# Kernel optimization log

Measured on AMD Instinct MI355X. Metric: run time of the kernel, lower is better.

The kernel has to match this reference:

```python
import jax, jax.numpy as jnp
import numpy as np


def _grid_sample(feat, grid):
    """Bilinear grid_sample, zeros padding, align_corners=False (torch default).
    feat: (B,C,H,W); grid: (B,Hg,Wg,2) normalized to [-1,1]. Returns (B,C,Hg,Wg)."""
    B, C, H, W = feat.shape
    gx, gy = grid[..., 0], grid[..., 1]
    ix = ((gx + 1.0) * W - 1.0) * 0.5
    iy = ((gy + 1.0) * H - 1.0) * 0.5
    x0 = jnp.floor(ix)
    y0 = jnp.floor(iy)
    wx = ix - x0
    wy = iy - y0

    def sample_one(f, x0, y0, wx, wy):
        def gather(xi, yi):
            valid = (xi >= 0) & (xi <= W - 1) & (yi >= 0) & (yi <= H - 1)
            xc = jnp.clip(xi, 0, W - 1).astype(jnp.int32)
            yc = jnp.clip(yi, 0, H - 1).astype(jnp.int32)
            return f[:, yc, xc] * valid[None].astype(f.dtype)
        v00 = gather(x0, y0)
        v01 = gather(x0 + 1, y0)
        v10 = gather(x0, y0 + 1)
        v11 = gather(x0 + 1, y0 + 1)
        return (v00 * (1 - wx) * (1 - wy) + v01 * wx * (1 - wy)
                + v10 * (1 - wx) * wy + v11 * wx * wy)

    return jax.vmap(sample_one)(feat, x0, y0, wx, wy)


def _homo_warp(src_feat, depth_hypo, src_K, src_c2w, ref_K, ref_c2w):
    """src_feat (B,C,H,W), depth_hypo (B,D,H,W) -> warped (B,C,D,H,W)."""
    B, C, H, W = src_feat.shape
    D = depth_hypo.shape[1]
    src_w2c = jnp.linalg.inv(src_c2w)
    ref_w2c = jnp.linalg.inv(ref_c2w)
    # Faithful to torch: clone w2c, overwrite top-left 3x3 with intrinsics.
    src_K4 = src_w2c.at[:, :3, :3].set(src_K)
    ref_K4 = ref_w2c.at[:, :3, :3].set(ref_K)
    src_proj = src_K4 @ src_w2c
    ref_proj = ref_K4 @ ref_w2c
    proj = src_proj @ jnp.linalg.inv(ref_proj)
    rot = proj[:, :3, :3]                      # (B,3,3)
    trans = proj[:, :3, 3]                     # (B,3)
    y, x = jnp.meshgrid(jnp.arange(H, dtype=src_feat.dtype),
                        jnp.arange(W, dtype=src_feat.dtype), indexing='ij')
    xyz = jnp.stack([x.ravel(), y.ravel(), jnp.ones(H * W, src_feat.dtype)], 0)  # (3,HW)
    rot_xyz = jnp.einsum('bij,jn->bin', rot, xyz)                                 # (B,3,HW)
    d = depth_hypo.reshape(B, 1, D, H * W)
    proj_xyz = rot_xyz[:, :, None, :] * d + trans[:, :, None, None]               # (B,3,D,HW)
    proj_xy = proj_xyz[:, :2] / proj_xyz[:, 2:3]
    gx = proj_xy[:, 0] / ((W - 1) / 2.0) - 1.0
    gy = proj_xy[:, 1] / ((H - 1) / 2.0) - 1.0
    grid = jax.lax.stop_gradient(jnp.stack([gx, gy], -1).reshape(B, D * H, W, 2))
    warped = _grid_sample(src_feat, grid)                                          # (B,C,D*H,W)
    return warped.reshape(B, C, D, H, W)


def _unfold5(x):
    """F.unfold(k=5,p=2) reshaped: (B,C,H,W) -> (B,C,25,H,W); k = dy*5+dx."""
    B, C, H, W = x.shape
    xp = jnp.pad(x, ((0, 0), (0, 0), (2, 2), (2, 2)))
    return jnp.stack([xp[:, :, dy:dy + H, dx:dx + W]
                      for dy in range(5) for dx in range(5)], axis=2)


def _cost_aggregation(cost, ref_feat, depth_hypo):
    B, D, H, W = cost.shape
    CENTER = 12  # index of 5x5 window center
    cost_nb = _unfold5(cost)                                           # (B,D,25,H,W)
    depth_nb = jax.lax.stop_gradient(_unfold5(depth_hypo))             # (B,D,25,H,W)
    w_depth = jax.nn.softmax(-jnp.abs(depth_nb - depth_nb[:, :, CENTER:CENTER + 1]), axis=2)
    feat_nb = jax.lax.stop_gradient(_unfold5(ref_feat))                # (B,C,25,H,W)
    w_feat = jnp.sum(feat_nb[:, :, CENTER:CENTER + 1] * feat_nb, axis=1, keepdims=True)
    w_feat = jax.nn.softmax(jnp.broadcast_to(w_feat, (B, D, 25, H, W)), axis=2)
    weight = jax.lax.stop_gradient(jax.nn.softmax(w_depth * w_feat, axis=2))
    return jnp.sum(cost_nb * weight, axis=2)                           # (B,D,H,W)


def setup_inputs() -> dict:
    key = jax.random.key(0)
    V, B, C, D, H, W = 3, 2, 32, 32, 128, 160
    k1, k2 = jax.random.split(key)
    features = jax.random.normal(k1, (V, B, C, H, W), jnp.float32)
    uncertainty = jax.random.normal(k2, (B, H, W), jnp.float32)
    K = np.array([[float(W), 0.0, (W - 1) / 2.0],
                  [0.0, float(W), (H - 1) / 2.0],
                  [0.0, 0.0, 1.0]], np.float32)
    intrinsics = np.broadcast_to(K, (V, B, 3, 3)).copy()
    c2w = np.tile(np.eye(4, dtype=np.float32), (V, B, 1, 1))
    for v in range(1, V):
        ang = 0.05 * v
        R = np.array([[np.cos(ang), 0.0, np.sin(ang)],
                      [0.0, 1.0, 0.0],
                      [-np.sin(ang), 0.0, np.cos(ang)]], np.float32)
        c2w[v, :, :3, :3] = R
        c2w[v, :, 0, 3] = 0.2 * v
    depth_vals = jnp.asarray(np.linspace(2.0, 10.0, D, dtype=np.float32))
    depth_hypo = jnp.broadcast_to(depth_vals[None, :, None, None], (B, D, H, W)) + 0.0
    return {
        'features': features,
        'intrinsics': jnp.asarray(intrinsics),
        'cam_to_world': jnp.asarray(c2w),
        'depth_hypo': depth_hypo,
        'uncertainty': uncertainty,
    }


def reference(features, intrinsics, cam_to_world, depth_hypo, uncertainty):
    ref_feat = features[0]                                             # (B,C,H,W)
    V = features.shape[0]
    unc = jax.nn.sigmoid(uncertainty)[:, None, None]                   # (B,1,1,H,W)
    pairwise = []
    for v in range(1, V):
        warped = _homo_warp(features[v], depth_hypo,
                            intrinsics[v], cam_to_world[v],
                            intrinsics[0], cam_to_world[0])            # (B,C,D,H,W)
        c = jnp.sum(ref_feat[:, :, None] * warped, axis=1, keepdims=True)  # correlation
        pairwise.append(c * unc)
    cost = jnp.min(jnp.stack(pairwise, 0), axis=0)[:, 0]               # (B,D,H,W)
    agg = _cost_aggregation(cost, ref_feat, depth_hypo)
    prob = jax.nn.softmax(agg, axis=1)
    return jnp.sum(prob * depth_hypo, axis=1)                          # (B,H,W)
```

## Files before the change

kernel.cpp:

```cpp
#include <hip/hip_runtime.h>
#include <hip/hip_fp16.h>
#include <math.h>

#define V_ 3
#define B_ 2
#define C_ 32
#define D_ 32
#define H_ 128
#define W_ 160
#define HW_ (H_*W_)
#define NPIX_ (B_*H_*W_)
#define NCOST_ (B_*D_*H_*W_)

struct H8 { __half2 h[4]; };

__device__ __forceinline__ void inv4(const double* m, double* o) {
    double inv[16];
    inv[0]  =  m[5]*m[10]*m[15] - m[5]*m[11]*m[14] - m[9]*m[6]*m[15] + m[9]*m[7]*m[14] + m[13]*m[6]*m[11] - m[13]*m[7]*m[10];
    inv[4]  = -m[4]*m[10]*m[15] + m[4]*m[11]*m[14] + m[8]*m[6]*m[15] - m[8]*m[7]*m[14] - m[12]*m[6]*m[11] + m[12]*m[7]*m[10];
    inv[8]  =  m[4]*m[9]*m[15]  - m[4]*m[11]*m[13] - m[8]*m[5]*m[15] + m[8]*m[7]*m[13] + m[12]*m[5]*m[11] - m[12]*m[7]*m[9];
    inv[12] = -m[4]*m[9]*m[14]  + m[4]*m[10]*m[13] + m[8]*m[5]*m[14] - m[8]*m[6]*m[13] - m[12]*m[5]*m[10] + m[12]*m[6]*m[9];
    inv[1]  = -m[1]*m[10]*m[15] + m[1]*m[11]*m[14] + m[9]*m[2]*m[15] - m[9]*m[3]*m[14] - m[13]*m[2]*m[11] + m[13]*m[3]*m[10];
    inv[5]  =  m[0]*m[10]*m[15] - m[0]*m[11]*m[14] - m[8]*m[2]*m[15] + m[8]*m[3]*m[14] + m[12]*m[2]*m[11] - m[12]*m[3]*m[10];
    inv[9]  = -m[0]*m[9]*m[15]  + m[0]*m[11]*m[13] + m[8]*m[1]*m[15] - m[8]*m[3]*m[13] - m[12]*m[1]*m[11] + m[12]*m[3]*m[9];
    inv[13] =  m[0]*m[9]*m[14]  - m[0]*m[10]*m[13] - m[8]*m[1]*m[14] + m[8]*m[2]*m[13] + m[12]*m[1]*m[10] - m[12]*m[2]*m[9];
    inv[2]  =  m[1]*m[6]*m[15]  - m[1]*m[7]*m[14]  - m[5]*m[2]*m[15] + m[5]*m[3]*m[14] + m[13]*m[2]*m[7]  - m[13]*m[3]*m[6];
    inv[6]  = -m[0]*m[6]*m[15]  + m[0]*m[7]*m[14]  + m[4]*m[2]*m[15] - m[4]*m[3]*m[14] - m[12]*m[2]*m[7]  + m[12]*m[3]*m[6];
    inv[10] =  m[0]*m[5]*m[15]  - m[0]*m[7]*m[13]  - m[4]*m[1]*m[15] + m[4]*m[3]*m[13] + m[12]*m[1]*m[7]  - m[12]*m[3]*m[5];
    inv[14] = -m[0]*m[5]*m[14]  + m[0]*m[6]*m[13]  + m[4]*m[1]*m[14] - m[4]*m[2]*m[13] - m[12]*m[1]*m[6]  + m[12]*m[2]*m[5];
    inv[3]  = -m[1]*m[6]*m[11]  + m[1]*m[7]*m[10]  + m[5]*m[2]*m[11] - m[5]*m[3]*m[10] - m[9]*m[2]*m[7]   + m[9]*m[3]*m[6];
    inv[7]  =  m[0]*m[6]*m[11]  - m[0]*m[7]*m[10]  - m[4]*m[2]*m[11] + m[4]*m[3]*m[10] + m[8]*m[2]*m[7]   - m[8]*m[3]*m[6];
    inv[11] = -m[0]*m[5]*m[11]  + m[0]*m[7]*m[9]   + m[4]*m[1]*m[11] - m[4]*m[3]*m[9]  - m[8]*m[1]*m[7]   + m[8]*m[3]*m[5];
    inv[15] =  m[0]*m[5]*m[10]  - m[0]*m[6]*m[9]   - m[4]*m[1]*m[10] + m[4]*m[2]*m[9]  + m[8]*m[1]*m[6]   - m[8]*m[2]*m[5];
    double det = m[0]*inv[0] + m[1]*inv[4] + m[2]*inv[8] + m[3]*inv[12];
    det = 1.0 / det;
    for (int i = 0; i < 16; i++) o[i] = inv[i] * det;
}

__device__ __forceinline__ void mm4(const double* A, const double* Bm, double* Cm) {
    for (int r = 0; r < 4; r++)
        for (int c = 0; c < 4; c++) {
            double s = 0.0;
            for (int k = 0; k < 4; k++) s += A[r*4+k] * Bm[k*4+c];
            Cm[r*4+c] = s;
        }
}

__global__ void __launch_bounds__(256) transproj_kernel(const float* __restrict__ feat,
                                                        const float* __restrict__ K,
                                                        const float* __restrict__ c2w,
                                                        float* __restrict__ refT,
                                                        __half* __restrict__ fh,
                                                        float* __restrict__ proj_out) {
    int bid = blockIdx.x;
    int tid = threadIdx.x;
    if (bid == V_ * B_ * H_ * (W_ / 32)) {
        int t = tid;
        if (t >= (V_-1) * B_) return;
        int vv = t / B_;
        int b  = t % B_;
        int v  = vv + 1;
        double sc[16], rc[16];
        for (int i = 0; i < 16; i++) {
            sc[i] = (double)c2w[((size_t)v * B_ + b) * 16 + i];
            rc[i] = (double)c2w[((size_t)0 * B_ + b) * 16 + i];
        }
        double sw[16], rw[16];
        inv4(sc, sw);
        inv4(rc, rw);
        double sK[16], rK[16];
        for (int i = 0; i < 16; i++) { sK[i] = sw[i]; rK[i] = rw[i]; }
        for (int r = 0; r < 3; r++)
            for (int c = 0; c < 3; c++) {
                sK[r*4+c] = (double)K[((size_t)v * B_ + b) * 9 + r*3 + c];
                rK[r*4+c] = (double)K[((size_t)0 * B_ + b) * 9 + r*3 + c];
            }
        double sp[16], rp[16], rpi[16], P[16];
        mm4(sK, sw, sp);
        mm4(rK, rw, rp);
        inv4(rp, rpi);
        mm4(sp, rpi, P);
        float* o = proj_out + (size_t)t * 12;
        for (int r = 0; r < 3; r++)
            for (int c = 0; c < 3; c++) o[r*3+c] = (float)P[r*4+c];
        for (int r = 0; r < 3; r++) o[9+r] = (float)P[r*4+3];
        return;
    }
    __shared__ float lds[32][33];
    int xt = bid % (W_ / 32);
    int y  = (bid / (W_ / 32)) % H_;
    int vb = bid / ((W_ / 32) * H_);
    int v = vb >> 1, b = vb & 1;
    int x0 = xt * 32;
    int xl = tid & 31;
    int ch = tid >> 5;
#pragma unroll
    for (int it = 0; it < 4; it++) {
        int c = it * 8 + ch;
        lds[c][xl] = feat[((size_t)(vb * C_ + c) * H_ + y) * W_ + x0 + xl];
    }
    __syncthreads();
    int c4 = tid & 7;
    int xw = tid >> 3;
    float4 o;
    o.x = lds[c4*4+0][xw];
    o.y = lds[c4*4+1][xw];
    o.z = lds[c4*4+2][xw];
    o.w = lds[c4*4+3][xw];
    size_t pix = (size_t)(b * H_ + y) * W_ + x0 + xw;
    if (v == 0) {
        *(float4*)(refT + pix * C_ + c4 * 4) = o;
    } else {
        uint2 st;
        __half2 p0 = __floats2half2_rn(o.x, o.y);
        __half2 p1 = __floats2half2_rn(o.z, o.w);
        st.x = *(unsigned int*)&p0;
        st.y = *(unsigned int*)&p1;
        size_t dst = ((size_t)((v - 1) * B_ + b) * HW_ + (y * W_ + x0 + xw));
        *(uint2*)((unsigned short*)fh + dst * C_ + c4 * 4) = st;
    }
}

union SmemU {
    struct { float4 lw[2][256]; int4 lo[2][256]; } c;
    float4 wbox[5 * 36 * 8];
};
__global__ void __launch_bounds__(256, 4) costwfeat_kernel(const float* __restrict__ refT,
                                                           const __half* __restrict__ fh,
                                                           const float* __restrict__ depth,
                                                           const float* __restrict__ unc,
                                                           const float* __restrict__ proj,
                                                           float* __restrict__ cost,
                                                           float* __restrict__ wfeat) {
    __shared__ SmemU sm;
    int tid = threadIdx.x;
    int bid = blockIdx.x;
    const int blocksPerDt = NPIX_ / 32;

    if (bid < 4 * blocksPerDt) {
        int dt      = bid / blocksPerDt;
        int pixbase = (bid % blocksPerDt) * 32;
        int d0 = dt * 8;
        {
            int pixl = tid & 31;
            int dl   = tid >> 5;
            int pix = pixbase + pixl;
            int x = pix % W_;
            int y = (pix / W_) % H_;
            int b = pix / HW_;
            float dep = depth[((b * D_ + d0 + dl) * H_ + y) * W_ + x];
            float fx = (float)x, fy = (float)y;
#pragma unroll
            for (int v = 0; v < 2; v++) {
                const float* P = proj + ((size_t)v * B_ + b) * 12;
                float rx = P[0]*fx + P[1]*fy + P[2];
                float ry = P[3]*fx + P[4]*fy + P[5];
                float rz = P[6]*fx + P[7]*fy + P[8];
                float px = rx * dep + P[9];
                float py = ry * dep + P[10];
                float pz = rz * dep + P[11];
                float inv_pz = 1.0f / pz;
                float t0 = px * inv_pz;
                float t1 = py * inv_pz;
                float gx = t0 / ((W_ - 1) * 0.5f) - 1.0f;
                float gy = t1 / ((H_ - 1) * 0.5f) - 1.0f;
                float ix = ((gx + 1.0f) * W_ - 1.0f) * 0.5f;
                float iy = ((gy + 1.0f) * H_ - 1.0f) * 0.5f;
                float x0f = floorf(ix), y0f = floorf(iy);
                float wx = ix - x0f, wy = iy - y0f;
                int x0 = (int)x0f, y0 = (int)y0f;
                int x1 = x0 + 1, y1 = y0 + 1;
                bool vx0 = (x0 >= 0) && (x0 <= W_ - 1);
                bool vx1 = (x1 >= 0) && (x1 <= W_ - 1);
                bool vy0 = (y0 >= 0) && (y0 <= H_ - 1);
                bool vy1 = (y1 >= 0) && (y1 <= H_ - 1);
                float4 w;
                w.x = (vx0 && vy0) ? (1.0f - wx) * (1.0f - wy) : 0.0f;
                w.y = (vx1 && vy0) ? wx * (1.0f - wy) : 0.0f;
                w.z = (vx0 && vy1) ? (1.0f - wx) * wy : 0.0f;
                w.w = (vx1 && vy1) ? wx * wy : 0.0f;
                int xc0 = min(max(x0, 0), W_ - 1), xc1 = min(max(x1, 0), W_ - 1);
                int yc0 = min(max(y0, 0), H_ - 1), yc1 = min(max(y1, 0), H_ - 1);
                int4 o;
                o.x = (yc0 * W_ + xc0) << 6;
                o.y = (yc0 * W_ + xc1) << 6;
                o.z = (yc1 * W_ + xc0) << 6;
                o.w = (yc1 * W_ + xc1) << 6;
                sm.c.lw[v][tid] = w;
                sm.c.lo[v][tid] = o;
            }
        }
        __syncthreads();

        int c8 = tid & 3;
        int g  = (tid >> 2) & 31;
        int h  = tid >> 7;
        int pix = pixbase + g;
        int x = pix % W_;
        int y = (pix / W_) % H_;
        int b = pix / HW_;

        const float4* rT4 = (const float4*)refT;
        const float4 r0 = rT4[(size_t)pix * 8 + c8 * 2];
        const float4 r1 = rT4[(size_t)pix * 8 + c8 * 2 + 1];
        const char* bA = (const char*)fh + ((size_t)(0 * B_ + b) * HW_) * 64 + c8 * 16;
        const char* bB = (const char*)fh + ((size_t)(1 * B_ + b) * HW_) * 64 + c8 * 16;

        float u = unc[pix];
        float sig = 1.0f / (1.0f + __expf(-u));

        float myres = 0.0f;
#pragma unroll
        for (int i = 0; i < 4; i++) {
            int e = (h * 4 + i) * 32 + g;
            float pv[2];
#pragma unroll
            for (int v = 0; v < 2; v++) {
                float4 Wt = sm.c.lw[v][e];
                int4   Of = sm.c.lo[v][e];
                const char* base = v ? bB : bA;
                H8 a  = *(const H8*)(base + Of.x);
                H8 bq = *(const H8*)(base + Of.y);
                H8 cq = *(const H8*)(base + Of.z);
                H8 eq = *(const H8*)(base + Of.w);
                __half2 w0 = __float2half2_rn(Wt.x);
                __half2 w1 = __float2half2_rn(Wt.y);
                __half2 w2 = __float2half2_rn(Wt.z);
                __half2 w3 = __float2half2_rn(Wt.w);
                __half2 acc0 = __hmul2(w0, a.h[0]);
                __half2 acc1 = __hmul2(w0, a.h[1]);
                __half2 acc2 = __hmul2(w0, a.h[2]);
                __half2 acc3 = __hmul2(w0, a.h[3]);
                acc0 = __hfma2(w1, bq.h[0], acc0);
                acc1 = __hfma2(w1, bq.h[1], acc1);
                acc2 = __hfma2(w1, bq.h[2], acc2);
                acc3 = __hfma2(w1, bq.h[3], acc3);
                acc0 = __hfma2(w2, cq.h[0], acc0);
                acc1 = __hfma2(w2, cq.h[1], acc1);
                acc2 = __hfma2(w2, cq.h[2], acc2);
                acc3 = __hfma2(w2, cq.h[3], acc3);
                acc0 = __hfma2(w3, eq.h[0], acc0);
                acc1 = __hfma2(w3, eq.h[1], acc1);
                acc2 = __hfma2(w3, eq.h[2], acc2);
                acc3 = __hfma2(w3, eq.h[3], acc3);
                float2 f0 = __half22float2(acc0);
                float2 f1 = __half22float2(acc1);
                float2 f2 = __half22float2(acc2);
                float2 f3 = __half22float2(acc3);
                float p = r0.x*f0.x + r0.y*f0.y + r0.z*f1.x + r0.w*f1.y
                        + r1.x*f2.x + r1.y*f2.y + r1.z*f3.x + r1.w*f3.y;
                p += __shfl_xor(p, 1);
                p += __shfl_xor(p, 2);
                pv[v] = p;
            }
            float r = fminf(pv[0], pv[1]) * sig;
            if (c8 == i) myres = r;
        }
        cost[((b * D_ + d0 + h * 4 + c8) * H_ + y) * W_ + x] = myres;
    } else {
        int wbid = bid - 4 * blocksPerDt;
        int g  = tid >> 3;
        int c4 = tid & 7;
        int pixbase = wbid * 32;
        int x0 = pixbase % W_;
        int yb = (pixbase / W_) % H_;
        int b  = pixbase / HW_;
        const float4* rT4 = (const float4*)refT;

        for (int e = tid; e < 5 * 36 * 8; e += 256) {
            int ent = e >> 3, q = e & 7;
            int ry = ent / 36, rx = ent - ry * 36;
            int yy = yb + ry - 2, xx = x0 + rx - 2;
            float4 val = make_float4(0.f, 0.f, 0.f, 0.f);
            if (yy >= 0 && yy < H_ && xx >= 0 && xx < W_)
                val = rT4[(size_t)((b * H_ + yy) * W_ + xx) * 8 + q];
            sm.wbox[e] = val;
        }
        __syncthreads();

        const float4 r = sm.wbox[(2 * 36 + g + 2) * 8 + c4];
        float logit[25];
#pragma unroll
        for (int k = 0; k < 25; k++) {
            int dy = k / 5, dx = k % 5;
            float4 q = sm.wbox[(dy * 36 + g + dx) * 8 + c4];
            float p = r.x*q.x + r.y*q.y + r.z*q.z + r.w*q.w;
            p += __shfl_xor(p, 1);
            p += __shfl_xor(p, 2);
            p += __shfl_xor(p, 4);
            logit[k] = p;
        }
        float m = logit[0];
#pragma unroll
        for (int k = 1; k < 25; k++) m = fmaxf(m, logit[k]);
        float s = 0.0f;
#pragma unroll
        for (int k = 0; k < 25; k++) { logit[k] = __expf(logit[k] - m); s += logit[k]; }
        float inv_s = 1.0f / s;
        int pix = pixbase + g;
#pragma unroll
        for (int t = 0; t < 3; t++) {
            int k = c4 + 8 * t;
            wfeat[(size_t)k * NPIX_ + pix] = logit[k] * inv_s;
        }
        if (c4 == 0) wfeat[(size_t)24 * NPIX_ + pix] = logit[24] * inv_s;
    }
}

__global__ void __launch_bounds__(256, 4) aggfinal_kernel(const float* __restrict__ depth,
                                                          const float* __restrict__ cost,
                                                          const float* __restrict__ wfeat,
                                                          float* __restrict__ out) {
    __shared__ float wf[25][33];
    __shared__ float aval[D_][33];
    __shared__ float dval[D_][33];
    int tid = threadIdx.x;
    int xl = tid & 31;
    int dl = tid >> 5;
    int bid = blockIdx.x;
    int xt = bid % (W_ / 32);
    int by = bid / (W_ / 32);
    int y = by % H_;
    int b = by / H_;
    int x = xt * 32 + xl;

    for (int li = tid; li < 25 * 32; li += 256) {
        int k  = li >> 5;
        int pp = li & 31;
        wf[k][pp] = wfeat[(size_t)k * NPIX_ + (b * H_ + y) * W_ + xt * 32 + pp];
    }
    __syncthreads();

#pragma unroll
    for (int i = 0; i < 4; i++) {
        int d = dl * 4 + i;
        size_t dslice = (size_t)(b * D_ + d) * HW_;
        float dc = depth[dslice + y * W_ + x];

        float wd[25];
        float s1 = 0.0f;
#pragma unroll
        for (int k = 0; k < 25; k++) {
            int dy = k / 5 - 2, dx = k % 5 - 2;
            int ny = y + dy, nx = x + dx;
            bool ok = (ny >= 0 && ny < H_ && nx >= 0 && nx < W_);
            float nd = ok ? depth[dslice + ny * W_ + nx] : 0.0f;
            float e = __expf(-fabsf(nd - dc));
            wd[k] = e;
            s1 += e;
        }
        float inv_s1 = 1.0f / s1;

        float s2 = 0.0f;
        float acc = 0.0f;
#pragma unroll
        for (int k = 0; k < 25; k++) {
            float e = __expf((wd[k] * inv_s1) * wf[k][xl]);
            s2 += e;
            int dy = k / 5 - 2, dx = k % 5 - 2;
            int ny = y + dy, nx = x + dx;
            bool ok = (ny >= 0 && ny < H_ && nx >= 0 && nx < W_);
            float cv = ok ? cost[dslice + ny * W_ + nx] : 0.0f;
            acc += cv * e;
        }
        aval[d][xl] = acc / s2;
        dval[d][xl] = dc;
    }
    __syncthreads();

    if (tid < 32) {
        float m = -1e30f;
#pragma unroll
        for (int dd = 0; dd < D_; dd++) m = fmaxf(m, aval[dd][tid]);
        float s = 0.0f, ws = 0.0f;
#pragma unroll
        for (int dd = 0; dd < D_; dd++) {
            float e = __expf(aval[dd][tid] - m);
            s += e;
            ws += e * dval[dd][tid];
        }
        out[(b * H_ + y) * W_ + xt * 32 + tid] = ws / s;
    }
}

extern "C" void kernel_launch(void* const* d_in, const int* in_sizes, int n_in,
                              void* d_out, int out_size, void* d_ws, size_t ws_size,
                              hipStream_t stream) {
    const float* features = (const float*)d_in[0];
    const float* intr     = (const float*)d_in[1];
    const float* c2w      = (const float*)d_in[2];
    const float* depth    = (const float*)d_in[3];
    const float* unc      = (const float*)d_in[4];
    float* out = (float*)d_out;

    float*  ws    = (float*)d_ws;
    float*  refT  = ws;
    __half* fh    = (__half*)(refT + (size_t)B_ * HW_ * C_);
    float*  cost  = (float*)(fh + (size_t)2 * B_ * HW_ * C_);
    float*  wfeat = cost + NCOST_;
    float*  proj  = wfeat + (size_t)25 * NPIX_;

    hipLaunchKernelGGL(transproj_kernel, dim3(V_ * B_ * H_ * (W_ / 32) + 1), dim3(256), 0, stream,
                       features, intr, c2w, refT, fh, proj);
    hipLaunchKernelGGL(costwfeat_kernel, dim3((NPIX_ * 4) / 32 + NPIX_ / 32), dim3(256), 0, stream,
                       refT, fh, depth, unc, proj, cost, wfeat);
    hipLaunchKernelGGL(aggfinal_kernel, dim3(NPIX_ / 32), dim3(256), 0, stream,
                       depth, cost, wfeat, out);
}
```

Baseline: 70.44 us.

## Store reference features in fp16 and use packed fdot2 for correlations

The reference view's features are now stored as fp16 in the same transposed buffer as the source views, not as fp32. The cost kernel computes per-corner dot products with the v_dot2 fp32-accumulate instruction and applies the bilinear weights afterwards, instead of interpolating in fp16 and then dotting in fp32. The aggregation-weight path also reads fp16 neighbours into a halved shared-memory box, and the launch bound raises target occupancy to 8 blocks per unit. This cuts memory traffic and shared memory but lowers precision of the reference features, and the correlation changes from one interpolated dot product to four dot products.

Measured after the change: 74.23 us. 5.4% more time.

```diff
diff --git a/kernel.cpp b/kernel.cpp
--- a/kernel.cpp
+++ b/kernel.cpp
@@ -13,6 +13,17 @@
 #define NCOST_ (B_*D_*H_*W_)
 
 struct H8 { __half2 h[4]; };
+struct H4 { __half2 h[2]; };
+
+typedef _Float16 hv2 __attribute__((ext_vector_type(2)));
+__device__ __forceinline__ float fdot2f(__half2 a, __half2 b, float c) {
+#if __has_builtin(__builtin_amdgcn_fdot2)
+    return __builtin_amdgcn_fdot2(*(hv2*)&a, *(hv2*)&b, c, false);
+#else
+    float2 fa = __half22float2(a), fb = __half22float2(b);
+    return c + fa.x * fb.x + fa.y * fb.y;
+#endif
+}
 
 __device__ __forceinline__ void inv4(const double* m, double* o) {
     double inv[16];
@@ -49,7 +60,6 @@
 __global__ void __launch_bounds__(256) transproj_kernel(const float* __restrict__ feat,
                                                         const float* __restrict__ K,
                                                         const float* __restrict__ c2w,
-                                                        float* __restrict__ refT,
                                                         __half* __restrict__ fh,
                                                         float* __restrict__ proj_out) {
     int bid = blockIdx.x;
@@ -90,7 +100,6 @@
     int xt = bid % (W_ / 32);
     int y  = (bid / (W_ / 32)) % H_;
     int vb = bid / ((W_ / 32) * H_);
-    int v = vb >> 1, b = vb & 1;
     int x0 = xt * 32;
     int xl = tid & 31;
     int ch = tid >> 5;
@@ -107,26 +116,20 @@
     o.y = lds[c4*4+1][xw];
     o.z = lds[c4*4+2][xw];
     o.w = lds[c4*4+3][xw];
-    size_t pix = (size_t)(b * H_ + y) * W_ + x0 + xw;
-    if (v == 0) {
-        *(float4*)(refT + pix * C_ + c4 * 4) = o;
-    } else {
-        uint2 st;
-        __half2 p0 = __floats2half2_rn(o.x, o.y);
-        __half2 p1 = __floats2half2_rn(o.z, o.w);
-        st.x = *(unsigned int*)&p0;
-        st.y = *(unsigned int*)&p1;
-        size_t dst = ((size_t)((v - 1) * B_ + b) * HW_ + (y * W_ + x0 + xw));
-        *(uint2*)((unsigned short*)fh + dst * C_ + c4 * 4) = st;
-    }
+    uint2 st;
+    __half2 p0 = __floats2half2_rn(o.x, o.y);
+    __half2 p1 = __floats2half2_rn(o.z, o.w);
+    st.x = *(unsigned int*)&p0;
+    st.y = *(unsigned int*)&p1;
+    size_t dst = (size_t)vb * HW_ + (y * W_ + x0 + xw);
+    *(uint2*)((unsigned short*)fh + dst * C_ + c4 * 4) = st;
 }
 
 union SmemU {
     struct { float4 lw[2][256]; int4 lo[2][256]; } c;
-    float4 wbox[5 * 36 * 8];
+    H4 wbox2[5 * 36 * 8];
 };
-__global__ void __launch_bounds__(256, 4) costwfeat_kernel(const float* __restrict__ refT,
-                                                           const __half* __restrict__ fh,
+__global__ void __launch_bounds__(256, 8) costwfeat_kernel(const __half* __restrict__ fh,
                                                            const float* __restrict__ depth,
                                                            const float* __restrict__ unc,
                                                            const float* __restrict__ proj,
@@ -200,11 +203,9 @@
         int y = (pix / W_) % H_;
         int b = pix / HW_;
 
-        const float4* rT4 = (const float4*)refT;
-        const float4 r0 = rT4[(size_t)pix * 8 + c8 * 2];
-        const float4 r1 = rT4[(size_t)pix * 8 + c8 * 2 + 1];
-        const char* bA = (const char*)fh + ((size_t)(0 * B_ + b) * HW_) * 64 + c8 * 16;
-        const char* bB = (const char*)fh + ((size_t)(1 * B_ + b) * HW_) * 64 + c8 * 16;
+        const H8 rh = *(const H8*)((const char*)fh + (size_t)pix * 64 + c8 * 16);
+        const char* bA = (const char*)fh + ((size_t)(NPIX_ + b * HW_)) * 64 + c8 * 16;
+        const char* bB = (const char*)fh + ((size_t)(2 * NPIX_ + b * HW_)) * 64 + c8 * 16;
 
         float u = unc[pix];
         float sig = 1.0f / (1.0f + __expf(-u));
@@ -223,32 +224,15 @@
                 H8 bq = *(const H8*)(base + Of.y);
                 H8 cq = *(const H8*)(base + Of.z);
                 H8 eq = *(const H8*)(base + Of.w);
-                __half2 w0 = __float2half2_rn(Wt.x);
-                __half2 w1 = __float2half2_rn(Wt.y);
-                __half2 w2 = __float2half2_rn(Wt.z);
-                __half2 w3 = __float2half2_rn(Wt.w);
-                __half2 acc0 = __hmul2(w0, a.h[0]);
-                __half2 acc1 = __hmul2(w0, a.h[1]);
-                __half2 acc2 = __hmul2(w0, a.h[2]);
-                __half2 acc3 = __hmul2(w0, a.h[3]);
-                acc0 = __hfma2(w1, bq.h[0], acc0);
-                acc1 = __hfma2(w1, bq.h[1], acc1);
-                acc2 = __hfma2(w1, bq.h[2], acc2);
-                acc3 = __hfma2(w1, bq.h[3], acc3);
-                acc0 = __hfma2(w2, cq.h[0], acc0);
-                acc1 = __hfma2(w2, cq.h[1], acc1);
-                acc2 = __hfma2(w2, cq.h[2], acc2);
-                acc3 = __hfma2(w2, cq.h[3], acc3);
-                acc0 = __hfma2(w3, eq.h[0], acc0);
-                acc1 = __hfma2(w3, eq.h[1], acc1);
-                acc2 = __hfma2(w3, eq.h[2], acc2);
-                acc3 = __hfma2(w3, eq.h[3], acc3);
-                float2 f0 = __half22float2(acc0);
-                float2 f1 = __half22float2(acc1);
-                float2 f2 = __half22float2(acc2);
-                float2 f3 = __half22float2(acc3);
-                float p = r0.x*f0.x + r0.y*f0.y + r0.z*f1.x + r0.w*f1.y
-                        + r1.x*f2.x + r1.y*f2.y + r1.z*f3.x + r1.w*f3.y;
+                float d00 = 0.f, d01 = 0.f, d10 = 0.f, d11 = 0.f;
+#pragma unroll
+                for (int j = 0; j < 4; j++) {
+                    d00 = fdot2f(rh.h[j], a.h[j],  d00);
+                    d01 = fdot2f(rh.h[j], bq.h[j], d01);
+                    d10 = fdot2f(rh.h[j], cq.h[j], d10);
+                    d11 = fdot2f(rh.h[j], eq.h[j], d11);
+                }
+                float p = Wt.x*d00 + Wt.y*d01 + Wt.z*d10 + Wt.w*d11;
                 p += __shfl_xor(p, 1);
                 p += __shfl_xor(p, 2);
                 pv[v] = p;
@@ -265,26 +249,28 @@
         int x0 = pixbase % W_;
         int yb = (pixbase / W_) % H_;
         int b  = pixbase / HW_;
-        const float4* rT4 = (const float4*)refT;
 
         for (int e = tid; e < 5 * 36 * 8; e += 256) {
             int ent = e >> 3, q = e & 7;
             int ry = ent / 36, rx = ent - ry * 36;
             int yy = yb + ry - 2, xx = x0 + rx - 2;
-            float4 val = make_float4(0.f, 0.f, 0.f, 0.f);
+            H4 val;
+            val.h[0] = __floats2half2_rn(0.f, 0.f);
+            val.h[1] = val.h[0];
             if (yy >= 0 && yy < H_ && xx >= 0 && xx < W_)
-                val = rT4[(size_t)((b * H_ + yy) * W_ + xx) * 8 + q];
-            sm.wbox[e] = val;
+                val = *(const H4*)((const char*)fh + (size_t)(b * HW_ + yy * W_ + xx) * 64 + q * 8);
+            sm.wbox2[e] = val;
         }
         __syncthreads();
 
-        const float4 r = sm.wbox[(2 * 36 + g + 2) * 8 + c4];
+        const H4 r = sm.wbox2[(2 * 36 + g + 2) * 8 + c4];
         float logit[25];
 #pragma unroll
         for (int k = 0; k < 25; k++) {
             int dy = k / 5, dx = k % 5;
-            float4 q = sm.wbox[(dy * 36 + g + dx) * 8 + c4];
-            float p = r.x*q.x + r.y*q.y + r.z*q.z + r.w*q.w;
+            H4 q = sm.wbox2[(dy * 36 + g + dx) * 8 + c4];
+            float p = fdot2f(r.h[0], q.h[0], 0.0f);
+            p = fdot2f(r.h[1], q.h[1], p);
             p += __shfl_xor(p, 1);
             p += __shfl_xor(p, 2);
             p += __shfl_xor(p, 4);
@@ -394,16 +380,15 @@
     float* out = (float*)d_out;
 
     float*  ws    = (float*)d_ws;
-    float*  refT  = ws;
-    __half* fh    = (__half*)(refT + (size_t)B_ * HW_ * C_);
-    float*  cost  = (float*)(fh + (size_t)2 * B_ * HW_ * C_);
+    __half* fh    = (__half*)ws;
+    float*  cost  = (float*)(fh + (size_t)3 * B_ * HW_ * C_);
     float*  wfeat = cost + NCOST_;
     float*  proj  = wfeat + (size_t)25 * NPIX_;
 
     hipLaunchKernelGGL(transproj_kernel, dim3(V_ * B_ * H_ * (W_ / 32) + 1), dim3(256), 0, stream,
-                       features, intr, c2w, refT, fh, proj);
+                       features, intr, c2w, fh, proj);
     hipLaunchKernelGGL(costwfeat_kernel, dim3((NPIX_ * 4) / 32 + NPIX_ / 32), dim3(256), 0, stream,
-                       refT, fh, depth, unc, proj, cost, wfeat);
+                       fh, depth, unc, proj, cost, wfeat);
     hipLaunchKernelGGL(aggfinal_kernel, dim3(NPIX_ / 32), dim3(256), 0, stream,
                        depth, cost, wfeat, out);
 }
```
